# Performance work log

Measured on AMD Instinct MI355X. Metric: run time of the kernel, lower is better.

The kernel has to match this reference:

```python
import jax, jax.numpy as jnp
import numpy as np


def setup_inputs() -> dict:
    key = jax.random.key(0)
    B, S, D, H = 4, 2048, 1024, 16
    hd = D // H
    ks = jax.random.split(key, 11)
    sc = 1.0 / np.sqrt(D)
    return {
        "keys": jax.random.normal(ks[0], (B, S, D), jnp.float32),
        "queries": jax.random.normal(ks[1], (B, S, D), jnp.float32),
        "values": jax.random.normal(ks[2], (B, S, D), jnp.float32),
        "Wq": jax.random.normal(ks[3], (H, D, hd), jnp.float32) * sc,
        "bq": jax.random.normal(ks[4], (H, hd), jnp.float32) * 0.02,
        "Wk": jax.random.normal(ks[5], (H, D, hd), jnp.float32) * sc,
        "bk": jax.random.normal(ks[6], (H, hd), jnp.float32) * 0.02,
        "Wv": jax.random.normal(ks[7], (H, D, hd), jnp.float32) * sc,
        "bv": jax.random.normal(ks[8], (H, hd), jnp.float32) * 0.02,
        "Wo": jax.random.normal(ks[9], (D, D), jnp.float32) * sc,
        "bo": jax.random.normal(ks[10], (D,), jnp.float32) * 0.02,
    }


def reference(keys, queries, values, Wq, bq, Wk, bk, Wv, bv, Wo, bo):
    # Per-head linear projections: [B,S,D] x [H,D,hd] -> [B,H,S,hd]
    q = jnp.einsum("bsd,hde->bhse", queries, Wq) + bq[None, :, None, :]
    k = jnp.einsum("bsd,hde->bhse", keys, Wk) + bk[None, :, None, :]
    v = jnp.einsum("bsd,hde->bhse", values, Wv) + bv[None, :, None, :]

    hd = q.shape[-1]
    S = q.shape[2]
    scores = jnp.einsum("bhse,bhte->bhst", q, k) / jnp.sqrt(jnp.float32(hd))
    causal = jnp.tril(jnp.ones((S, S), dtype=bool))  # tril buffer
    scores = jnp.where(causal[None, None, :, :], scores, -jnp.inf)
    attn = jax.nn.softmax(scores, axis=-1)  # dropout p=0 (eval)

    o = jnp.einsum("bhst,bhte->bhse", attn, v)  # [B,H,S,hd]
    # concat heads -> [B,S,H*hd]
    o = o.transpose(0, 2, 1, 3).reshape(o.shape[0], S, -1)
    return o @ Wo + bo
```

## Files before the change

kernel.cpp:

```cpp
#include <hip/hip_runtime.h>
#include <stdint.h>

typedef unsigned short u16;
typedef __attribute__((ext_vector_type(4))) float f32x4;
typedef __attribute__((ext_vector_type(8))) short bfrag;

static __device__ __forceinline__ u16 f2bf(float f) {
  union { float f; uint32_t u; } v; v.f = f;
  return (u16)((v.u + 0x7fffu + ((v.u >> 16) & 1u)) >> 16);
}
static __device__ __forceinline__ uint32_t cvtpk(float lo, float hi) {
  uint32_t r;
  asm("v_cvt_pk_bf16_f32 %0, %1, %2" : "=v"(r) : "v"(lo), "v"(hi));
  return r;
}
static __device__ __forceinline__ uint32_t pk2bf(float lo, float hi) {
  union { float f; uint32_t u; } a, b; a.f = lo; b.f = hi;
  return __builtin_amdgcn_perm(b.u + 0x8000u, a.u + 0x8000u, 0x07060302u);
}

#define GLOAD16(gp, lp)                                              \
  __builtin_amdgcn_global_load_lds(                                  \
      (const __attribute__((address_space(1))) uint32_t*)(gp),       \
      (__attribute__((address_space(3))) uint32_t*)(lp), 16, 0, 0)

__global__ __launch_bounds__(256) void pack_w_hde(const float* __restrict__ W,
                                                  u16* __restrict__ Wt) {
  __shared__ float tile[64][65];
  const int h = blockIdx.y, k0 = blockIdx.x * 64;
  const int tid = threadIdx.x;
#pragma unroll
  for (int j = 0; j < 4; ++j) {
    int idx = tid + j * 256;
    int rr = idx >> 4, c4 = (idx & 15) * 4;
    const float4 v = *(const float4*)(W + (size_t)h * 65536 + (size_t)(k0 + rr) * 64 + c4);
    tile[rr][c4 + 0] = v.x; tile[rr][c4 + 1] = v.y;
    tile[rr][c4 + 2] = v.z; tile[rr][c4 + 3] = v.w;
  }
  __syncthreads();
#pragma unroll
  for (int j = 0; j < 4; ++j) {
    int idx = tid + j * 256;
    int ee = idx >> 4, c4 = (idx & 15) * 4;
    uint2 u;
    u.x = f2bf(tile[c4 + 0][ee]) | ((uint32_t)f2bf(tile[c4 + 1][ee]) << 16);
    u.y = f2bf(tile[c4 + 2][ee]) | ((uint32_t)f2bf(tile[c4 + 3][ee]) << 16);
    *(uint2*)(Wt + (size_t)(h * 64 + ee) * 1024 + k0 + c4) = u;
  }
}

__global__ __launch_bounds__(256) void transpose_w(const float* __restrict__ W,
                                                   u16* __restrict__ Wt) {
  __shared__ float tile[64][65];
  const int k0 = blockIdx.x * 64, n0 = blockIdx.y * 64;
  const int tid = threadIdx.x;
#pragma unroll
  for (int j = 0; j < 4; ++j) {
    int idx = tid + j * 256;
    int rr = idx >> 4, c4 = (idx & 15) * 4;
    const float4 v = *(const float4*)(W + (size_t)(k0 + rr) * 1024 + n0 + c4);
    tile[rr][c4 + 0] = v.x; tile[rr][c4 + 1] = v.y;
    tile[rr][c4 + 2] = v.z; tile[rr][c4 + 3] = v.w;
  }
  __syncthreads();
#pragma unroll
  for (int j = 0; j < 4; ++j) {
    int idx = tid + j * 256;
    int ee = idx >> 4, c4 = (idx & 15) * 4;
    uint2 u;
    u.x = f2bf(tile[c4 + 0][ee]) | ((uint32_t)f2bf(tile[c4 + 1][ee]) << 16);
    u.y = f2bf(tile[c4 + 2][ee]) | ((uint32_t)f2bf(tile[c4 + 3][ee]) << 16);
    *(uint2*)(Wt + (size_t)(n0 + ee) * 1024 + k0 + c4) = u;
  }
}

__global__ __launch_bounds__(256) void gemm_qkv(
    const float* __restrict__ Aq, const float* __restrict__ Ak,
    const float* __restrict__ Avv, const u16* __restrict__ Bt,
    const float* __restrict__ bq, const float* __restrict__ bk,
    const float* __restrict__ bv,
    u16* __restrict__ Qb, u16* __restrict__ Kb, u16* __restrict__ Vt) {
  __shared__ u16 As[2][128 * 32];
  __shared__ u16 Bs[2][128 * 32];
  const int tid = threadIdx.x;
  const int n = blockIdx.x;
  const int xcd = n & 7, j = n >> 3;
  const int mb = xcd * 8 + (j & 7);
  const int nb = j >> 3;
  const int chunk = nb >> 3;
  const float* Af = (chunk == 0) ? Aq : (chunk == 1) ? Ak : Avv;
  const int wid = tid >> 6, lane = tid & 63;
  const int wr = wid >> 1, wc = wid & 1;
  const int g = lane >> 4, l15 = lane & 15;
  f32x4 acc[4][4] = {};

  const int bsrc = ((lane & 3) ^ ((lane >> 3) & 3)) * 8;
  const u16* Bg = Bt + (size_t)(nb * 128 + 2 * wid * 16 + (lane >> 2)) * 1024 + bsrc;
  const float* Ap = Af + (size_t)(mb * 128 + (tid >> 2)) * 1024 + (tid & 3) * 8;
  const int arow = tid >> 2;
  const int acs = (((tid & 3) ^ ((tid >> 3) & 3))) * 8;
  const int swzr = (l15 >> 1) & 3;

  float4 fa[2][2];
#pragma unroll
  for (int c = 0; c < 2; ++c) {
    fa[c][0] = *(const float4*)(Ap + (size_t)c * 64 * 1024);
    fa[c][1] = *(const float4*)(Ap + (size_t)c * 64 * 1024 + 4);
  }
#pragma unroll
  for (int c = 0; c < 2; ++c)
    GLOAD16(Bg + (size_t)c * 16 * 1024, &Bs[0][2 * wid * 512 + c * 512]);
#pragma unroll
  for (int c = 0; c < 2; ++c) {
    uint4 u;
    u.x = pk2bf(fa[c][0].x, fa[c][0].y); u.y = pk2bf(fa[c][0].z, fa[c][0].w);
    u.z = pk2bf(fa[c][1].x, fa[c][1].y); u.w = pk2bf(fa[c][1].z, fa[c][1].w);
    *(uint4*)&As[0][(arow + c * 64) * 32 + acs] = u;
  }
  __syncthreads();
  int cur = 0;
  for (int kk = 0; kk < 32; ++kk) {
    if (kk < 31) {
      const int kn = (kk + 1) * 32;
#pragma unroll
      for (int c = 0; c < 2; ++c) {
        fa[c][0] = *(const float4*)(Ap + (size_t)c * 64 * 1024 + kn);
        fa[c][1] = *(const float4*)(Ap + (size_t)c * 64 * 1024 + kn + 4);
      }
#pragma unroll
      for (int c = 0; c < 2; ++c)
        GLOAD16(Bg + (size_t)c * 16 * 1024 + kn, &Bs[cur ^ 1][2 * wid * 512 + c * 512]);
    }
    bfrag a[4], b[4];
#pragma unroll
    for (int m = 0; m < 4; ++m)
      a[m] = __builtin_bit_cast(bfrag,
          *(const uint4*)&As[cur][(wr * 64 + m * 16 + l15) * 32 + ((g ^ swzr)) * 8]);
#pragma unroll
    for (int nn = 0; nn < 4; ++nn)
      b[nn] = __builtin_bit_cast(bfrag,
          *(const uint4*)&Bs[cur][(wc * 64 + nn * 16 + l15) * 32 + ((g ^ swzr)) * 8]);
    __builtin_amdgcn_s_setprio(1);
#pragma unroll
    for (int m = 0; m < 4; ++m)
#pragma unroll
      for (int nn = 0; nn < 4; ++nn)
        acc[m][nn] = __builtin_amdgcn_mfma_f32_16x16x32_bf16(a[m], b[nn], acc[m][nn], 0, 0, 0);
    __builtin_amdgcn_s_setprio(0);
    if (kk < 31) {
#pragma unroll
      for (int c = 0; c < 2; ++c) {
        uint4 u;
        u.x = pk2bf(fa[c][0].x, fa[c][0].y); u.y = pk2bf(fa[c][0].z, fa[c][0].w);
        u.z = pk2bf(fa[c][1].x, fa[c][1].y); u.w = pk2bf(fa[c][1].z, fa[c][1].w);
        *(uint4*)&As[cur ^ 1][(arow + c * 64) * 32 + acs] = u;
      }
      __syncthreads();
      cur ^= 1;
    }
  }

  const int row0 = mb * 128 + wr * 64 + g * 4;
  const int cc0 = (nb & 7) * 128 + wc * 64 + l15;
  const float* bias = (chunk == 0) ? bq : (chunk == 1) ? bk : bv;
  const float qs = (chunk == 0) ? 0.125f : 1.0f;
#pragma unroll
  for (int m = 0; m < 4; ++m) {
#pragma unroll
    for (int nn = 0; nn < 4; ++nn) {
      const int row = row0 + m * 16;
      const int cc = cc0 + nn * 16;
      const float bcv = bias[cc];
      if (chunk < 2) {
        u16* dst = (chunk == 0) ? Qb : Kb;
#pragma unroll
        for (int r = 0; r < 4; ++r)
          dst[(size_t)(row + r) * 1024 + cc] = f2bf((acc[m][nn][r] + bcv) * qs);
      } else {
        u16 w[4];
#pragma unroll
        for (int r = 0; r < 4; ++r) w[r] = f2bf(acc[m][nn][r] + bcv);
        const size_t dst =
            ((size_t)((row >> 11) * 16 + (cc >> 6)) * 64 + (cc & 63)) * 2048 + (row & 2047);
        *(uint2*)(Vt + dst) = *(const uint2*)w;
      }
    }
  }
}

__global__ __launch_bounds__(256) void gemm_o(const u16* __restrict__ Abf,
                                              const u16* __restrict__ Bt,
                                              const float* __restrict__ bo,
                                              float* __restrict__ Of) {
  __shared__ u16 As[2][128 * 32];
  __shared__ u16 Bs[2][128 * 32];
  const int tid = threadIdx.x;
  const int n = blockIdx.x;
  const int xcd = n & 7, j = n >> 3;
  const int mb = xcd * 8 + (j & 7);
  const int nb = j >> 3;
  const int wid = tid >> 6, lane = tid & 63;
  const int wr = wid >> 1, wc = wid & 1;
  const int g = lane >> 4, l15 = lane & 15;
  f32x4 acc[4][4] = {};

  const int bsrc = ((lane & 3) ^ ((lane >> 3) & 3)) * 8;
  const int swzr = (l15 >> 1) & 3;
  const u16* Bg = Bt + (size_t)(nb * 128 + 2 * wid * 16 + (lane >> 2)) * 1024 + bsrc;
  const u16* Ag = Abf + (size_t)(mb * 128 + 2 * wid * 16 + (lane >> 2)) * 1024 + bsrc;

#pragma unroll
  for (int c = 0; c < 2; ++c) {
    GLOAD16(Ag + (size_t)c * 16 * 1024, &As[0][2 * wid * 512 + c * 512]);
    GLOAD16(Bg + (size_t)c * 16 * 1024, &Bs[0][2 * wid * 512 + c * 512]);
  }
  __syncthreads();
  int cur = 0;
  for (int kk = 0; kk < 32; ++kk) {
    if (kk < 31) {
      const int kn = (kk + 1) * 32;
#pragma unroll
      for (int c = 0; c < 2; ++c) {
        GLOAD16(Ag + (size_t)c * 16 * 1024 + kn, &As[cur ^ 1][2 * wid * 512 + c * 512]);
        GLOAD16(Bg + (size_t)c * 16 * 1024 + kn, &Bs[cur ^ 1][2 * wid * 512 + c * 512]);
      }
    }
    bfrag a[4], b[4];
#pragma unroll
    for (int m = 0; m < 4; ++m)
      a[m] = __builtin_bit_cast(bfrag,
          *(const uint4*)&As[cur][(wr * 64 + m * 16 + l15) * 32 + ((g ^ swzr)) * 8]);
#pragma unroll
    for (int nn = 0; nn < 4; ++nn)
      b[nn] = __builtin_bit_cast(bfrag,
          *(const uint4*)&Bs[cur][(wc * 64 + nn * 16 + l15) * 32 + ((g ^ swzr)) * 8]);
    __builtin_amdgcn_s_setprio(1);
#pragma unroll
    for (int m = 0; m < 4; ++m)
#pragma unroll
      for (int nn = 0; nn < 4; ++nn)
        acc[m][nn] = __builtin_amdgcn_mfma_f32_16x16x32_bf16(a[m], b[nn], acc[m][nn], 0, 0, 0);
    __builtin_amdgcn_s_setprio(0);
    if (kk < 31) { __syncthreads(); cur ^= 1; }
  }

  const int row0 = mb * 128 + wr * 64 + g * 4;
  const int col0 = nb * 128 + wc * 64 + l15;
#pragma unroll
  for (int m = 0; m < 4; ++m)
#pragma unroll
    for (int nn = 0; nn < 4; ++nn) {
      const int row = row0 + m * 16, col = col0 + nn * 16;
      const float bcv = bo[col];
#pragma unroll
      for (int r = 0; r < 4; ++r)
        Of[(size_t)(row + r) * 1024 + col] = acc[m][nn][r] + bcv;
    }
}

__global__ __launch_bounds__(512) void attn_fused(const u16* __restrict__ Qb,
                                                  const u16* __restrict__ Kb,
                                                  const u16* __restrict__ Vtg,
                                                  u16* __restrict__ Ob) {
  __shared__ u16 KV[2][2][4096];
  const int tid = threadIdx.x;
  const int wid = tid >> 6, lane = tid & 63;
  const int g = lane >> 4, l15 = lane & 15;
  const int n = blockIdx.x;
  const int half = n >> 8, idx = n & 255;
  const int xcd = idx & 7;
  const int bh = xcd * 8 + ((idx >> 3) & 7);
  const int grp = idx >> 6;
  const int u = half ? grp : (7 - grp);
  const int t = u * 8 + wid;
  const int b = bh >> 4, h = bh & 15;
  const size_t baserow = (size_t)b * 2048;
  const u16* Qg = Qb + baserow * 1024 + h * 64;
  const u16* Kg = Kb + baserow * 1024 + h * 64;
  const u16* Vg = Vtg + (size_t)bh * 64 * 2048;
  u16* Og = Ob + baserow * 1024 + h * 64;

  const int q0 = t * 32;
  const int qrow = q0 + l15;
  const int mysteps = (q0 >> 6) + 1;
  const int smax = 4 * u + 4;

  const int sr = tid >> 3;
  const int scc = (tid & 7) ^ (sr & 7);
  const u16* Kst = Kg + (size_t)sr * 1024 + scc * 8;
  const u16* Vst = Vg + (size_t)sr * 2048 + scc * 8;

  bfrag qa[2][2];
#pragma unroll
  for (int qf = 0; qf < 2; ++qf)
#pragma unroll
    for (int kh = 0; kh < 2; ++kh)
      qa[qf][kh] = __builtin_bit_cast(bfrag,
          *(const uint4*)(Qg + (size_t)(q0 + qf * 16 + l15) * 1024 + kh * 32 + g * 8));

  f32x4 accT[2][4] = {};
  float M[2] = {-1e30f, -1e30f}, Ll[2] = {0.f, 0.f};

  const int s0lane = ((g & 1) << 5) | l15;
  const int s1lane = s0lane + 16;
  const bool ghi = (g >= 2);
  const int swz = l15 & 7;

  GLOAD16(Kst, &KV[0][0][wid * 512]);
  GLOAD16(Vst, &KV[0][1][wid * 512]);
  __syncthreads();

  for (int s = 0; s < smax; ++s) {
    const int cb = s & 1;
    if (s + 1 < smax) {
      const size_t kn = (size_t)(s + 1) << 6;
      GLOAD16(Kst + kn * 1024, &KV[cb ^ 1][0][wid * 512]);
      GLOAD16(Vst + kn, &KV[cb ^ 1][1][wid * 512]);
    }
    if (s < mysteps) {
      const int kv0 = s << 6;
      const bool diag = (s == mysteps - 1);
      const u16* KB = &KV[cb][0][0];
      const u16* VB = &KV[cb][1][0];

      bfrag kb[2][4];
#pragma unroll
      for (int tt = 0; tt < 4; ++tt)
#pragma unroll
        for (int kh = 0; kh < 2; ++kh)
          kb[kh][tt] = __builtin_bit_cast(bfrag,
              *(const uint4*)&KB[(tt * 16 + l15) * 64 + (((kh << 2) | g) ^ swz) * 8]);

      f32x4 sc[2][4];
      __builtin_amdgcn_s_setprio(1);
#pragma unroll
      for (int qf = 0; qf < 2; ++qf)
#pragma unroll
        for (int tt = 0; tt < 4; ++tt) {
          f32x4 z = {0.f, 0.f, 0.f, 0.f};
          z = __builtin_amdgcn_mfma_f32_16x16x32_bf16(kb[0][tt], qa[qf][0], z, 0, 0, 0);
          z = __builtin_amdgcn_mfma_f32_16x16x32_bf16(kb[1][tt], qa[qf][1], z, 0, 0, 0);
          sc[qf][tt] = z;
        }
      __builtin_amdgcn_s_setprio(0);

      bfrag vb[2][4];
#pragma unroll
      for (int et = 0; et < 4; ++et)
#pragma unroll
        for (int kcb = 0; kcb < 2; ++kcb)
          vb[kcb][et] = __builtin_bit_cast(bfrag,
              *(const uint4*)&VB[(et * 16 + l15) * 64 + (((kcb << 2) | g) ^ swz) * 8]);

#pragma unroll
      for (int qf = 0; qf < 2; ++qf) {
        if (diag) {
          const int qq = qrow + qf * 16;
#pragma unroll
          for (int tt = 0; tt < 4; ++tt) {
            const int kvb = kv0 + tt * 16 + g * 4;
#pragma unroll
            for (int r = 0; r < 4; ++r)
              sc[qf][tt][r] = (kvb + r <= qq) ? sc[qf][tt][r] : -1e30f;
          }
        }
        float m01 = fmaxf(fmaxf(sc[qf][0][0], sc[qf][0][1]), fmaxf(sc[qf][0][2], sc[qf][0][3]));
        float m23 = fmaxf(fmaxf(sc[qf][1][0], sc[qf][1][1]), fmaxf(sc[qf][1][2], sc[qf][1][3]));
        float m45 = fmaxf(fmaxf(sc[qf][2][0], sc[qf][2][1]), fmaxf(sc[qf][2][2], sc[qf][2][3]));
        float m67 = fmaxf(fmaxf(sc[qf][3][0], sc[qf][3][1]), fmaxf(sc[qf][3][2], sc[qf][3][3]));
        const float mloc = fmaxf(fmaxf(m01, m23), fmaxf(m45, m67));
        if (!__all(mloc - M[qf] <= 6.0f)) {
          float mr = fmaxf(mloc, __shfl_xor(mloc, 16));
          mr = fmaxf(mr, __shfl_xor(mr, 32));
          const float Mn = fmaxf(M[qf], mr);
          const float cf = __expf(M[qf] - Mn);
          M[qf] = Mn;
          Ll[qf] *= cf;
#pragma unroll
          for (int et = 0; et < 4; ++et)
#pragma unroll
            for (int r = 0; r < 4; ++r) accT[qf][et][r] *= cf;
        }
        uint32_t pk[4][2];
        float ss = 0.f;
#pragma unroll
        for (int tt = 0; tt < 4; ++tt) {
          float p0 = __expf(sc[qf][tt][0] - M[qf]);
          float p1 = __expf(sc[qf][tt][1] - M[qf]);
          float p2 = __expf(sc[qf][tt][2] - M[qf]);
          float p3 = __expf(sc[qf][tt][3] - M[qf]);
          ss += (p0 + p1) + (p2 + p3);
          pk[tt][0] = cvtpk(p0, p1);
          pk[tt][1] = cvtpk(p2, p3);
        }
        Ll[qf] += ss;
        __builtin_amdgcn_s_setprio(1);
#pragma unroll
        for (int kcb = 0; kcb < 2; ++kcb) {
          const int lo = kcb * 2, hi = kcb * 2 + 1;
          const uint32_t a0 = __shfl(pk[lo][0], s0lane), b0 = __shfl(pk[hi][0], s0lane);
          const uint32_t a1 = __shfl(pk[lo][1], s0lane), b1 = __shfl(pk[hi][1], s0lane);
          const uint32_t a2 = __shfl(pk[lo][0], s1lane), b2 = __shfl(pk[hi][0], s1lane);
          const uint32_t a3 = __shfl(pk[lo][1], s1lane), b3 = __shfl(pk[hi][1], s1lane);
          uint4 uu;
          uu.x = ghi ? b0 : a0; uu.y = ghi ? b1 : a1;
          uu.z = ghi ? b2 : a2; uu.w = ghi ? b3 : a3;
          const bfrag pfrag = __builtin_bit_cast(bfrag, uu);
#pragma unroll
          for (int et = 0; et < 4; ++et)
            accT[qf][et] = __builtin_amdgcn_mfma_f32_16x16x32_bf16(vb[kcb][et], pfrag, accT[qf][et], 0, 0, 0);
        }
        __builtin_amdgcn_s_setprio(0);
      }
    }
    __syncthreads();
  }

#pragma unroll
  for (int qf = 0; qf < 2; ++qf) {
    float Ls = Ll[qf];
    Ls += __shfl_xor(Ls, 16);
    Ls += __shfl_xor(Ls, 32);
    const float inv = 1.f / Ls;
    u16* orow = Og + (size_t)(q0 + qf * 16 + l15) * 1024 + g * 4;
#pragma unroll
    for (int et = 0; et < 4; ++et) {
      uint2 w;
      w.x = cvtpk(accT[qf][et][0] * inv, accT[qf][et][1] * inv);
      w.y = cvtpk(accT[qf][et][2] * inv, accT[qf][et][3] * inv);
      *(uint2*)(orow + et * 16) = w;
    }
  }
}

extern "C" void kernel_launch(void* const* d_in, const int* in_sizes, int n_in,
                              void* d_out, int out_size, void* d_ws, size_t ws_size,
                              hipStream_t stream) {
  const float* keys    = (const float*)d_in[0];
  const float* queries = (const float*)d_in[1];
  const float* values  = (const float*)d_in[2];
  const float* Wq = (const float*)d_in[3];
  const float* bq = (const float*)d_in[4];
  const float* Wk = (const float*)d_in[5];
  const float* bk = (const float*)d_in[6];
  const float* Wv = (const float*)d_in[7];
  const float* bv = (const float*)d_in[8];
  const float* Wo = (const float*)d_in[9];
  const float* bo = (const float*)d_in[10];
  float* out = (float*)d_out;

  char* ws = (char*)d_ws;
  const size_t MB = 1u << 20;
  u16* Wqkvt = (u16*)(ws);
  u16* Wot   = (u16*)(ws + 6 * MB);
  u16* Qb    = (u16*)(ws + 8 * MB);
  u16* Kb    = (u16*)(ws + 24 * MB);
  u16* Vtg   = (u16*)(ws + 40 * MB);
  u16* Ob    = (u16*)(ws + 56 * MB);

  const dim3 pg(16, 16);
  pack_w_hde<<<pg, 256, 0, stream>>>(Wq, Wqkvt);
  pack_w_hde<<<pg, 256, 0, stream>>>(Wk, Wqkvt + (size_t)1024 * 1024);
  pack_w_hde<<<pg, 256, 0, stream>>>(Wv, Wqkvt + (size_t)2048 * 1024);
  transpose_w<<<pg, 256, 0, stream>>>(Wo, Wot);

  gemm_qkv<<<dim3(1536), 256, 0, stream>>>(queries, keys, values, Wqkvt,
                                           bq, bk, bv, Qb, Kb, Vtg);

  attn_fused<<<dim3(512), 512, 0, stream>>>(Qb, Kb, Vtg, Ob);

  gemm_o<<<dim3(512), 256, 0, stream>>>(Ob, Wot, bo, out);
}
```

Baseline: 197.5 us.

## Pre-convert QKV activations to bf16 and stream them with direct LDS loads

Adds a separate kernel that converts the fp32 query/key/value activations to bf16 once. A new QKV projection GEMM then loads bf16 A-tiles with global_load_lds async copies, the same way it loads B, in a double-buffered loop. This removes in-GEMM fp32 loading and conversion, where each A tile is reread by the eight column blocks of its chunk. In exchange it adds an extra pass writing and reading 48MB of bf16, and it only runs when the workspace is at least 104MB. Otherwise it falls back to the old kernel.

```diff
diff --git a/kernel.cpp b/kernel.cpp
--- a/kernel.cpp
+++ b/kernel.cpp
@@ -71,6 +71,111 @@
     u.x = f2bf(tile[c4 + 0][ee]) | ((uint32_t)f2bf(tile[c4 + 1][ee]) << 16);
     u.y = f2bf(tile[c4 + 2][ee]) | ((uint32_t)f2bf(tile[c4 + 3][ee]) << 16);
     *(uint2*)(Wt + (size_t)(n0 + ee) * 1024 + k0 + c4) = u;
+  }
+}
+
+__global__ __launch_bounds__(256) void conv_bf16(const float* __restrict__ q,
+                                                 const float* __restrict__ k,
+                                                 const float* __restrict__ v,
+                                                 u16* __restrict__ oq,
+                                                 u16* __restrict__ ok,
+                                                 u16* __restrict__ ov) {
+  const float* in = (blockIdx.y == 0) ? q : (blockIdx.y == 1) ? k : v;
+  u16* out = (blockIdx.y == 0) ? oq : (blockIdx.y == 1) ? ok : ov;
+  const size_t i = ((size_t)blockIdx.x * 256 + threadIdx.x) * 8;
+  const float4 f0 = *(const float4*)(in + i);
+  const float4 f1 = *(const float4*)(in + i + 4);
+  uint4 u;
+  u.x = pk2bf(f0.x, f0.y); u.y = pk2bf(f0.z, f0.w);
+  u.z = pk2bf(f1.x, f1.y); u.w = pk2bf(f1.z, f1.w);
+  *(uint4*)(out + i) = u;
+}
+
+__global__ __launch_bounds__(256) void gemm_qkvb(
+    const u16* __restrict__ cq, const u16* __restrict__ ck,
+    const u16* __restrict__ cv, const u16* __restrict__ Bt,
+    const float* __restrict__ bq, const float* __restrict__ bk,
+    const float* __restrict__ bv,
+    u16* __restrict__ Qb, u16* __restrict__ Kb, u16* __restrict__ Vt) {
+  __shared__ u16 As[2][128 * 32];
+  __shared__ u16 Bs[2][128 * 32];
+  const int tid = threadIdx.x;
+  const int n = blockIdx.x;
+  const int xcd = n & 7, j = n >> 3;
+  const int mb = xcd * 8 + (j & 7);
+  const int nb = j >> 3;
+  const int chunk = nb >> 3;
+  const u16* Abf = (chunk == 0) ? cq : (chunk == 1) ? ck : cv;
+  const int wid = tid >> 6, lane = tid & 63;
+  const int wr = wid >> 1, wc = wid & 1;
+  const int g = lane >> 4, l15 = lane & 15;
+  f32x4 acc[4][4] = {};
+
+  const int bsrc = ((lane & 3) ^ ((lane >> 3) & 3)) * 8;
+  const int swzr = (l15 >> 1) & 3;
+  const u16* Bg = Bt + (size_t)(nb * 128 + 2 * wid * 16 + (lane >> 2)) * 1024 + bsrc;
+  const u16* Ag = Abf + (size_t)(mb * 128 + 2 * wid * 16 + (lane >> 2)) * 1024 + bsrc;
+
+#pragma unroll
+  for (int c = 0; c < 2; ++c) {
+    GLOAD16(Ag + (size_t)c * 16 * 1024, &As[0][2 * wid * 512 + c * 512]);
+    GLOAD16(Bg + (size_t)c * 16 * 1024, &Bs[0][2 * wid * 512 + c * 512]);
+  }
+  __syncthreads();
+  int cur = 0;
+  for (int kk = 0; kk < 32; ++kk) {
+    if (kk < 31) {
+      const int kn = (kk + 1) * 32;
+#pragma unroll
+      for (int c = 0; c < 2; ++c) {
+        GLOAD16(Ag + (size_t)c * 16 * 1024 + kn, &As[cur ^ 1][2 * wid * 512 + c * 512]);
+        GLOAD16(Bg + (size_t)c * 16 * 1024 + kn, &Bs[cur ^ 1][2 * wid * 512 + c * 512]);
+      }
+    }
+    bfrag a[4], b[4];
+#pragma unroll
+    for (int m = 0; m < 4; ++m)
+      a[m] = __builtin_bit_cast(bfrag,
+          *(const uint4*)&As[cur][(wr * 64 + m * 16 + l15) * 32 + ((g ^ swzr)) * 8]);
+#pragma unroll
+    for (int nn = 0; nn < 4; ++nn)
+      b[nn] = __builtin_bit_cast(bfrag,
+          *(const uint4*)&Bs[cur][(wc * 64 + nn * 16 + l15) * 32 + ((g ^ swzr)) * 8]);
+    __builtin_amdgcn_s_setprio(1);
+#pragma unroll
+    for (int m = 0; m < 4; ++m)
+#pragma unroll
+      for (int nn = 0; nn < 4; ++nn)
+        acc[m][nn] = __builtin_amdgcn_mfma_f32_16x16x32_bf16(a[m], b[nn], acc[m][nn], 0, 0, 0);
+    __builtin_amdgcn_s_setprio(0);
+    if (kk < 31) { __syncthreads(); cur ^= 1; }
+  }
+
+  const int row0 = mb * 128 + wr * 64 + g * 4;
+  const int cc0 = (nb & 7) * 128 + wc * 64 + l15;
+  const float* bias = (chunk == 0) ? bq : (chunk == 1) ? bk : bv;
+  const float qs = (chunk == 0) ? 0.125f : 1.0f;
+#pragma unroll
+  for (int m = 0; m < 4; ++m) {
+#pragma unroll
+    for (int nn = 0; nn < 4; ++nn) {
+      const int row = row0 + m * 16;
+      const int cc = cc0 + nn * 16;
+      const float bcv = bias[cc];
+      if (chunk < 2) {
+        u16* dst = (chunk == 0) ? Qb : Kb;
+#pragma unroll
+        for (int r = 0; r < 4; ++r)
+          dst[(size_t)(row + r) * 1024 + cc] = f2bf((acc[m][nn][r] + bcv) * qs);
+      } else {
+        u16 w[4];
+#pragma unroll
+        for (int r = 0; r < 4; ++r) w[r] = f2bf(acc[m][nn][r] + bcv);
+        const size_t dst =
+            ((size_t)((row >> 11) * 16 + (cc >> 6)) * 64 + (cc & 63)) * 2048 + (row & 2047);
+        *(uint2*)(Vt + dst) = *(const uint2*)w;
+      }
+    }
   }
 }
 
@@ -457,6 +562,9 @@
   u16* Kb    = (u16*)(ws + 24 * MB);
   u16* Vtg   = (u16*)(ws + 40 * MB);
   u16* Ob    = (u16*)(ws + 56 * MB);
+  u16* cvQ   = (u16*)(ws + 56 * MB);
+  u16* cvK   = (u16*)(ws + 72 * MB);
+  u16* cvV   = (u16*)(ws + 88 * MB);
 
   const dim3 pg(16, 16);
   pack_w_hde<<<pg, 256, 0, stream>>>(Wq, Wqkvt);
@@ -464,8 +572,14 @@
   pack_w_hde<<<pg, 256, 0, stream>>>(Wv, Wqkvt + (size_t)2048 * 1024);
   transpose_w<<<pg, 256, 0, stream>>>(Wo, Wot);
 
-  gemm_qkv<<<dim3(1536), 256, 0, stream>>>(queries, keys, values, Wqkvt,
-                                           bq, bk, bv, Qb, Kb, Vtg);
+  if (ws_size >= 104 * MB) {
+    conv_bf16<<<dim3(4096, 3), 256, 0, stream>>>(queries, keys, values, cvQ, cvK, cvV);
+    gemm_qkvb<<<dim3(1536), 256, 0, stream>>>(cvQ, cvK, cvV, Wqkvt,
+                                              bq, bk, bv, Qb, Kb, Vtg);
+  } else {
+    gemm_qkv<<<dim3(1536), 256, 0, stream>>>(queries, keys, values, Wqkvt,
+                                             bq, bk, bv, Qb, Kb, Vtg);
+  }
 
   attn_fused<<<dim3(512), 512, 0, stream>>>(Qb, Kb, Vtg, Ob);
 
```

Measured after the change: 208.7 us. 1.06x slower.

## Compute two N-tiles per block in QKV GEMM to reuse fp32 A loads

Applied to the files above, without the earlier changes.

Each QKV GEMM block now computes two adjacent 128-column output tiles, sharing one converted A tile across both. This halves the global reads and bf16 conversions of the fp32 activations and halves the grid size. In exchange, accumulator registers and LDS per block double, which may reduce occupancy.

```diff
diff --git a/kernel.cpp b/kernel.cpp
--- a/kernel.cpp
+++ b/kernel.cpp
@@ -74,28 +74,37 @@
   }
 }
 
-__global__ __launch_bounds__(256) void gemm_qkv(
+__global__ __launch_bounds__(256) void gemm_qkv2(
     const float* __restrict__ Aq, const float* __restrict__ Ak,
     const float* __restrict__ Avv, const u16* __restrict__ Bt,
     const float* __restrict__ bq, const float* __restrict__ bk,
     const float* __restrict__ bv,
     u16* __restrict__ Qb, u16* __restrict__ Kb, u16* __restrict__ Vt) {
   __shared__ u16 As[2][128 * 32];
-  __shared__ u16 Bs[2][128 * 32];
+  __shared__ u16 Bs0[2][128 * 32];
+  __shared__ u16 Bs1[2][128 * 32];
   const int tid = threadIdx.x;
   const int n = blockIdx.x;
   const int xcd = n & 7, j = n >> 3;
   const int mb = xcd * 8 + (j & 7);
-  const int nb = j >> 3;
-  const int chunk = nb >> 3;
-  const float* Af = (chunk == 0) ? Aq : (chunk == 1) ? Ak : Avv;
+  const int jp = j >> 3;
+  const int nb0 = jp, nb1 = jp + 12;
+  const int chunk0 = nb0 >> 3, chunk1 = nb1 >> 3;
+  const float* Af0 = (chunk0 == 0) ? Aq : (chunk0 == 1) ? Ak : Avv;
+  const float* Af1 = (chunk1 == 0) ? Aq : (chunk1 == 1) ? Ak : Avv;
+  const int ch = jp >> 2, p2 = jp & 3;
+  const int nbA = ch * 8 + p2 * 2, nbB = nbA + 1;
+  const float* Af = (ch == 0) ? Aq : (ch == 1) ? Ak : Avv;
+
   const int wid = tid >> 6, lane = tid & 63;
   const int wr = wid >> 1, wc = wid & 1;
   const int g = lane >> 4, l15 = lane & 15;
-  f32x4 acc[4][4] = {};
+  f32x4 acc0[4][4] = {};
+  f32x4 acc1[4][4] = {};
 
   const int bsrc = ((lane & 3) ^ ((lane >> 3) & 3)) * 8;
-  const u16* Bg = Bt + (size_t)(nb * 128 + 2 * wid * 16 + (lane >> 2)) * 1024 + bsrc;
+  const u16* Bg0 = Bt + (size_t)(nbA * 128 + 2 * wid * 16 + (lane >> 2)) * 1024 + bsrc;
+  const u16* Bg1 = Bt + (size_t)(nbB * 128 + 2 * wid * 16 + (lane >> 2)) * 1024 + bsrc;
   const float* Ap = Af + (size_t)(mb * 128 + (tid >> 2)) * 1024 + (tid & 3) * 8;
   const int arow = tid >> 2;
   const int acs = (((tid & 3) ^ ((tid >> 3) & 3))) * 8;
@@ -108,8 +117,10 @@
     fa[c][1] = *(const float4*)(Ap + (size_t)c * 64 * 1024 + 4);
   }
 #pragma unroll
-  for (int c = 0; c < 2; ++c)
-    GLOAD16(Bg + (size_t)c * 16 * 1024, &Bs[0][2 * wid * 512 + c * 512]);
+  for (int c = 0; c < 2; ++c) {
+    GLOAD16(Bg0 + (size_t)c * 16 * 1024, &Bs0[0][2 * wid * 512 + c * 512]);
+    GLOAD16(Bg1 + (size_t)c * 16 * 1024, &Bs1[0][2 * wid * 512 + c * 512]);
+  }
 #pragma unroll
   for (int c = 0; c < 2; ++c) {
     uint4 u;
@@ -128,24 +139,31 @@
         fa[c][1] = *(const float4*)(Ap + (size_t)c * 64 * 1024 + kn + 4);
       }
 #pragma unroll
-      for (int c = 0; c < 2; ++c)
-        GLOAD16(Bg + (size_t)c * 16 * 1024 + kn, &Bs[cur ^ 1][2 * wid * 512 + c * 512]);
-    }
-    bfrag a[4], b[4];
+      for (int c = 0; c < 2; ++c) {
+        GLOAD16(Bg0 + (size_t)c * 16 * 1024 + kn, &Bs0[cur ^ 1][2 * wid * 512 + c * 512]);
+        GLOAD16(Bg1 + (size_t)c * 16 * 1024 + kn, &Bs1[cur ^ 1][2 * wid * 512 + c * 512]);
+      }
+    }
+    bfrag a[4], b0[4], b1[4];
 #pragma unroll
     for (int m = 0; m < 4; ++m)
       a[m] = __builtin_bit_cast(bfrag,
           *(const uint4*)&As[cur][(wr * 64 + m * 16 + l15) * 32 + ((g ^ swzr)) * 8]);
 #pragma unroll
-    for (int nn = 0; nn < 4; ++nn)
-      b[nn] = __builtin_bit_cast(bfrag,
-          *(const uint4*)&Bs[cur][(wc * 64 + nn * 16 + l15) * 32 + ((g ^ swzr)) * 8]);
+    for (int nn = 0; nn < 4; ++nn) {
+      b0[nn] = __builtin_bit_cast(bfrag,
+          *(const uint4*)&Bs0[cur][(wc * 64 + nn * 16 + l15) * 32 + ((g ^ swzr)) * 8]);
+      b1[nn] = __builtin_bit_cast(bfrag,
+          *(const uint4*)&Bs1[cur][(wc * 64 + nn * 16 + l15) * 32 + ((g ^ swzr)) * 8]);
+    }
     __builtin_amdgcn_s_setprio(1);
 #pragma unroll
     for (int m = 0; m < 4; ++m)
 #pragma unroll
-      for (int nn = 0; nn < 4; ++nn)
-        acc[m][nn] = __builtin_amdgcn_mfma_f32_16x16x32_bf16(a[m], b[nn], acc[m][nn], 0, 0, 0);
+      for (int nn = 0; nn < 4; ++nn) {
+        acc0[m][nn] = __builtin_amdgcn_mfma_f32_16x16x32_bf16(a[m], b0[nn], acc0[m][nn], 0, 0, 0);
+        acc1[m][nn] = __builtin_amdgcn_mfma_f32_16x16x32_bf16(a[m], b1[nn], acc1[m][nn], 0, 0, 0);
+      }
     __builtin_amdgcn_s_setprio(0);
     if (kk < 31) {
 #pragma unroll
@@ -161,28 +179,33 @@
   }
 
   const int row0 = mb * 128 + wr * 64 + g * 4;
-  const int cc0 = (nb & 7) * 128 + wc * 64 + l15;
-  const float* bias = (chunk == 0) ? bq : (chunk == 1) ? bk : bv;
-  const float qs = (chunk == 0) ? 0.125f : 1.0f;
-#pragma unroll
-  for (int m = 0; m < 4; ++m) {
-#pragma unroll
-    for (int nn = 0; nn < 4; ++nn) {
-      const int row = row0 + m * 16;
-      const int cc = cc0 + nn * 16;
-      const float bcv = bias[cc];
-      if (chunk < 2) {
-        u16* dst = (chunk == 0) ? Qb : Kb;
-#pragma unroll
-        for (int r = 0; r < 4; ++r)
-          dst[(size_t)(row + r) * 1024 + cc] = f2bf((acc[m][nn][r] + bcv) * qs);
-      } else {
-        u16 w[4];
-#pragma unroll
-        for (int r = 0; r < 4; ++r) w[r] = f2bf(acc[m][nn][r] + bcv);
-        const size_t dst =
-            ((size_t)((row >> 11) * 16 + (cc >> 6)) * 64 + (cc & 63)) * 2048 + (row & 2047);
-        *(uint2*)(Vt + dst) = *(const uint2*)w;
+  const float* bias = (ch == 0) ? bq : (ch == 1) ? bk : bv;
+  const float qs = (ch == 0) ? 0.125f : 1.0f;
+#pragma unroll
+  for (int tsel = 0; tsel < 2; ++tsel) {
+    const int nb = tsel ? nbB : nbA;
+    const int cc0 = (nb & 7) * 128 + wc * 64 + l15;
+#pragma unroll
+    for (int m = 0; m < 4; ++m) {
+#pragma unroll
+      for (int nn = 0; nn < 4; ++nn) {
+        const f32x4 av = tsel ? acc1[m][nn] : acc0[m][nn];
+        const int row = row0 + m * 16;
+        const int cc = cc0 + nn * 16;
+        const float bcv = bias[cc];
+        if (ch < 2) {
+          u16* dst = (ch == 0) ? Qb : Kb;
+#pragma unroll
+          for (int r = 0; r < 4; ++r)
+            dst[(size_t)(row + r) * 1024 + cc] = f2bf((av[r] + bcv) * qs);
+        } else {
+          u16 w[4];
+#pragma unroll
+          for (int r = 0; r < 4; ++r) w[r] = f2bf(av[r] + bcv);
+          const size_t dst =
+              ((size_t)((row >> 11) * 16 + (cc >> 6)) * 64 + (cc & 63)) * 2048 + (row & 2047);
+          *(uint2*)(Vt + dst) = *(const uint2*)w;
+        }
       }
     }
   }
@@ -464,7 +487,7 @@
   pack_w_hde<<<pg, 256, 0, stream>>>(Wv, Wqkvt + (size_t)2048 * 1024);
   transpose_w<<<pg, 256, 0, stream>>>(Wo, Wot);
 
-  gemm_qkv<<<dim3(1536), 256, 0, stream>>>(queries, keys, values, Wqkvt,
+  gemm_qkv2<<<dim3(768), 256, 0, stream>>>(queries, keys, values, Wqkvt,
                                            bq, bk, bv, Qb, Kb, Vtg);
 
   attn_fused<<<dim3(512), 512, 0, stream>>>(Qb, Kb, Vtg, Ob);
```

Result: slower. 259.6 us (+31.4%).
